# Kernel optimization log

Measured on AMD Instinct MI355X. Metric: run time of the kernel, lower is better.

The kernel has to match this reference:

```python
import jax, jax.numpy as jnp
import numpy as np

T, N, E, H = 10, 2048, 32768, 256
EPS = 1e-12  # F.normalize eps
COORDS_WEIGHT = 1.0


def setup_inputs() -> dict:
    key = jax.random.key(0)
    ks = jax.random.split(key, 16)

    def lin_w(k, fan_in, fan_out, gain=1.0):
        return (jax.random.normal(k, (fan_in, fan_out), jnp.float32)
                * gain / np.sqrt(fan_in)).astype(jnp.float32)

    return {
        "x": jax.random.normal(ks[0], (T, N, 4, 3), jnp.float32),
        "h": jax.random.normal(ks[1], (T, N, H), jnp.float32),
        "others": jax.random.normal(ks[2], (T, N, H), jnp.float32),
        # edge_mlp: Linear(2H+16 -> H), ReLU, Linear(H -> H), ReLU
        "We1": lin_w(ks[3], 2 * H + 16, H), "be1": jnp.zeros((H,), jnp.float32),
        "We2": lin_w(ks[4], H, H), "be2": jnp.zeros((H,), jnp.float32),
        # node_mlp: Linear(H + H + H -> H), ReLU, Linear(H -> H)
        "Wn1": lin_w(ks[5], 3 * H, H), "bn1": jnp.zeros((H,), jnp.float32),
        "Wn2": lin_w(ks[6], H, H), "bn2": jnp.zeros((H,), jnp.float32),
        # coord_mlp: Linear(H -> H), ReLU, Linear(H -> 1, bias=False, xavier gain 0.001)
        "Wc1": lin_w(ks[7], H, H), "bc1": jnp.zeros((H,), jnp.float32),
        "Wc2": lin_w(ks[8], H, 1, gain=0.001),
        "edge_index": jax.random.randint(ks[9], (2, E), 0, N, jnp.int64),
    }


def reference(x, h, others, We1, be1, We2, be2, Wn1, bn1, Wn2, bn2,
              Wc1, bc1, Wc2, edge_index):
    row, col = edge_index[0], edge_index[1]
    n_nodes = x.shape[1]

    # coord2radial (vectorized over the per-timestep python loop)
    coord_diff = x[:, row] - x[:, col]                      # [T,E,4,3]
    gram = jnp.einsum('tejd,tekd->tejk', coord_diff, coord_diff)
    gram = gram.reshape(gram.shape[0], gram.shape[1], 16)   # [T,E,16]
    radial = gram / jnp.maximum(
        jnp.linalg.norm(gram, axis=-1, keepdims=True), EPS)

    # edge_model: cat([source, target, radial]) -> MLP
    edge_in = jnp.concatenate([h[:, row], h[:, col], radial], axis=-1)
    e = jax.nn.relu(edge_in @ We1 + be1)
    e = jax.nn.relu(e @ We2 + be2)                          # [T,E,H]

    # coord_model: trans = coord_diff * coord_mlp(edge_feat)
    m = jax.nn.relu(e @ Wc1 + bc1) @ Wc2                    # [T,E,1]
    trans = coord_diff * m[..., None]                       # [T,E,4,3]

    seg_sum = lambda a: jax.vmap(
        lambda v: jax.ops.segment_sum(v, row, num_segments=n_nodes))(a)
    counts = jax.ops.segment_sum(
        jnp.ones((row.shape[0],), x.dtype), row, num_segments=n_nodes)
    counts = jnp.maximum(counts, 1.0)

    f = (seg_sum(trans) / counts[None, :, None, None]) * COORDS_WEIGHT
    coord_out = x + f                                       # [T,N,4,3]

    # node_model: agg = segment_sum(edge_feat, row); cat([others, h, agg])
    agg = seg_sum(e)                                        # [T,N,H]
    node_in = jnp.concatenate([others, h, agg], axis=-1)    # [T,N,3H]
    n_out = jax.nn.relu(node_in @ Wn1 + bn1) @ Wn2 + bn2
    h_out = h + n_out                                       # recurrent residual
    return h_out, coord_out
```

## Files before the change

kernel.cpp:

```cpp
#include <hip/hip_runtime.h>
#include <hip/hip_bf16.h>
#include <stdint.h>

#define TT 10
#define NN 2048
#define EE 32768
#define HH 256

typedef short bf16x8 __attribute__((ext_vector_type(8)));
typedef float f32x4 __attribute__((ext_vector_type(4)));

__device__ __forceinline__ float b2f(unsigned short u) {
    unsigned int x = ((unsigned int)u) << 16;
    return __builtin_bit_cast(float, x);
}
__device__ __forceinline__ unsigned short f2b(float f) {
    unsigned int x = __builtin_bit_cast(unsigned int, f);
    unsigned int r = x + 0x7FFFu + ((x >> 16) & 1u);
    return (unsigned short)(r >> 16);
}

#define GLOAD_LDS16(g, l)                                                      \
    __builtin_amdgcn_global_load_lds(                                          \
        (const __attribute__((address_space(1))) void*)(g),                    \
        (__attribute__((address_space(3))) void*)(l), 16, 0, 0)


__global__ void cvt_bf16_kernel(const float* __restrict__ in,
                                unsigned short* __restrict__ out, int n) {
    int i = blockIdx.x * blockDim.x + threadIdx.x;
    int stride = gridDim.x * blockDim.x;
    for (; i < n; i += stride) out[i] = f2b(in[i]);
}

__global__ void transpose_w_kernel(const float* __restrict__ W,
                                   unsigned short* __restrict__ Wt, int K, int KPAD) {
    int idx = blockIdx.x * blockDim.x + threadIdx.x;
    if (idx >= 256 * KPAD) return;
    int n = idx / KPAD, k = idx - n * KPAD;
    Wt[idx] = (k < K) ? f2b(W[k * 256 + n]) : (unsigned short)0;
}

__global__ void zero_f32_kernel(float* __restrict__ p, int n) {
    int i = blockIdx.x * blockDim.x + threadIdx.x;
    int stride = gridDim.x * blockDim.x;
    for (; i < n; i += stride) p[i] = 0.0f;
}

__global__ void count_kernel(const int* __restrict__ rows, int* __restrict__ counts) {
    int e = blockIdx.x * blockDim.x + threadIdx.x;
    if (e < EE) atomicAdd(&counts[rows[e]], 1);
}

__global__ __launch_bounds__(256) void scan_kernel(const int* __restrict__ counts,
                                                   int* __restrict__ boff) {
    __shared__ int part[256];
    int tid = threadIdx.x;
    int base = tid * 8;
    int local[8];
    int s = 0;
#pragma unroll
    for (int i = 0; i < 8; ++i) { local[i] = s; s += counts[base + i]; }
    part[tid] = s;
    __syncthreads();
    for (int offd = 1; offd < 256; offd <<= 1) {
        int v = (tid >= offd) ? part[tid - offd] : 0;
        __syncthreads();
        part[tid] += v;
        __syncthreads();
    }
    int pbase = (tid == 0) ? 0 : part[tid - 1];
#pragma unroll
    for (int i = 0; i < 8; ++i) boff[base + i] = pbase + local[i];
    if (tid == 255) boff[2048] = pbase + s;
}

__global__ void scatter_kernel(const int* __restrict__ rows, const int* __restrict__ cols,
                               const int* __restrict__ boff, int* __restrict__ cursor,
                               int* __restrict__ rs, int* __restrict__ cs) {
    int e = blockIdx.x * blockDim.x + threadIdx.x;
    if (e < EE) {
        int r = rows[e];
        int pos = boff[r] + atomicAdd(&cursor[r], 1);
        rs[pos] = r;
        cs[pos] = cols[e];
    }
}


__device__ __forceinline__ void stageB(const unsigned short* __restrict__ Wt,
                                       int KPAD, int k0, int tid, int w,
                                       unsigned short* Bs) {
    int trow = tid >> 3;
    int sk8 = ((tid & 7) ^ (trow & 7)) * 8;
#pragma unroll
    for (int i = 0; i < 8; ++i) {
        int row = i * 32 + trow;
        GLOAD_LDS16(Wt + (size_t)row * KPAD + k0 + sk8, Bs + i * 2048 + w * 512);
    }
}

__device__ __forceinline__ void mfma_step(const unsigned short* As,
                                          const unsigned short* Bs,
                                          int w, int lr, int lq, f32x4 acc[4][4]) {
    int xs = (lr & 7) << 3;
#pragma unroll
    for (int kk = 0; kk < 64; kk += 32) {
        bf16x8 a[4], b[4];
        int pc = (kk + lq * 8) ^ xs;
#pragma unroll
        for (int m = 0; m < 4; ++m)
            a[m] = *reinterpret_cast<const bf16x8*>(As + (m * 16 + lr) * 64 + pc);
#pragma unroll
        for (int n = 0; n < 4; ++n)
            b[n] = *reinterpret_cast<const bf16x8*>(
                Bs + (w * 64 + n * 16 + lr) * 64 + pc);
#pragma unroll
        for (int m = 0; m < 4; ++m)
#pragma unroll
            for (int n = 0; n < 4; ++n)
                acc[m][n] = __builtin_amdgcn_mfma_f32_16x16x32_bf16(
                    a[m], b[n], acc[m][n], 0, 0, 0);
    }
}

__device__ __forceinline__ void mfma_step_es(const unsigned short* Es,
                                             const unsigned short* Bs, int k0,
                                             int w, int lr, int lq, f32x4 acc[4][4]) {
    int xs = (lr & 7) << 3;
#pragma unroll
    for (int kk = 0; kk < 64; kk += 32) {
        bf16x8 a[4], b[4];
        int lcol = kk + lq * 8;
#pragma unroll
        for (int m = 0; m < 4; ++m)
            a[m] = *reinterpret_cast<const bf16x8*>(
                Es + (m * 16 + lr) * 256 + ((k0 + lcol) ^ xs));
#pragma unroll
        for (int n = 0; n < 4; ++n)
            b[n] = *reinterpret_cast<const bf16x8*>(
                Bs + (w * 64 + n * 16 + lr) * 64 + (lcol ^ xs));
#pragma unroll
        for (int m = 0; m < 4; ++m)
#pragma unroll
            for (int n = 0; n < 4; ++n)
                acc[m][n] = __builtin_amdgcn_mfma_f32_16x16x32_bf16(
                    a[m], b[n], acc[m][n], 0, 0, 0);
    }
}

__global__ __launch_bounds__(256, 2) void edge_mega_kernel(
    const float* __restrict__ x, const unsigned short* __restrict__ hb,
    const unsigned short* __restrict__ We1t, const float* __restrict__ be1,
    const unsigned short* __restrict__ We2t, const float* __restrict__ be2,
    const unsigned short* __restrict__ Wc1t, const float* __restrict__ bc1,
    const float* __restrict__ Wc2,
    const int* __restrict__ rs, const int* __restrict__ cs,
    float* __restrict__ aggf, float* __restrict__ csum) {
    __shared__ unsigned short As[64 * 64];
    __shared__ unsigned short Bs[256 * 64];
    __shared__ unsigned short Es[64 * 256];
    __shared__ float CDs[64][12];
    __shared__ unsigned short Rs[64][16];
    __shared__ float Ms[64][4];

    int tid = threadIdx.x;
    int lane = tid & 63, w = tid >> 6;
    int lr = lane & 15, lq = lane >> 4;
    int blockRow = blockIdx.x * 64;
    int tt = blockRow >> 15;
    int sb = blockRow & (EE - 1);

    if (tid < 64) {
        int s = sb + tid;
        int r = rs[s], c = cs[s];
        const float* xr = x + ((size_t)tt * NN + r) * 12;
        const float* xc = x + ((size_t)tt * NN + c) * 12;
        float cd[12];
#pragma unroll
        for (int i = 0; i < 12; ++i) {
            cd[i] = xr[i] - xc[i];
            CDs[tid][i] = cd[i];
        }
        float g[16], ss = 0.f;
#pragma unroll
        for (int j = 0; j < 4; ++j)
#pragma unroll
            for (int k = 0; k < 4; ++k) {
                float v = cd[j * 3] * cd[k * 3] + cd[j * 3 + 1] * cd[k * 3 + 1] +
                          cd[j * 3 + 2] * cd[k * 3 + 2];
                g[j * 4 + k] = v;
                ss += v * v;
            }
        float inv = 1.f / fmaxf(sqrtf(ss), 1e-12f);
#pragma unroll
        for (int i = 0; i < 16; ++i) Rs[tid][i] = f2b(g[i] * inv);
    }

    int trow = tid >> 3;
    int sk8 = ((tid & 7) ^ (trow & 7)) * 8;
    const unsigned short *hr0, *hc0, *hr1, *hc1;
    {
        int s0 = sb + trow;
        int s1 = sb + 32 + trow;
        hr0 = hb + ((size_t)tt * NN + rs[s0]) * 256 + sk8;
        hc0 = hb + ((size_t)tt * NN + cs[s0]) * 256 + sk8 - 256;
        hr1 = hb + ((size_t)tt * NN + rs[s1]) * 256 + sk8;
        hc1 = hb + ((size_t)tt * NN + cs[s1]) * 256 + sk8 - 256;
    }

    __syncthreads();

    f32x4 acc[4][4];
#pragma unroll
    for (int m = 0; m < 4; ++m)
#pragma unroll
        for (int n = 0; n < 4; ++n) acc[m][n] = (f32x4){0.f, 0.f, 0.f, 0.f};

#pragma unroll 1
    for (int k0 = 0; k0 < 512; k0 += 64) {
        const unsigned short* s0 = (k0 < 256) ? hr0 + k0 : hc0 + k0;
        const unsigned short* s1 = (k0 < 256) ? hr1 + k0 : hc1 + k0;
        GLOAD_LDS16(s0, As + w * 512);
        GLOAD_LDS16(s1, As + 2048 + w * 512);
        stageB(We1t, 576, k0, tid, w, Bs);
        __syncthreads();
        mfma_step(As, Bs, w, lr, lq, acc);
        __syncthreads();
    }
    {
#pragma unroll
        for (int j = 0; j < 2; ++j) {
            int row = j * 32 + trow;
            int lseg = (tid & 7) ^ (row & 7);
            bf16x8 v = {};
            if (lseg < 2) {
#pragma unroll
                for (int ii = 0; ii < 8; ++ii)
                    v[ii] = (short)Rs[row][lseg * 8 + ii];
            }
            *reinterpret_cast<bf16x8*>(As + row * 64 + (tid & 7) * 8) = v;
        }
        stageB(We1t, 576, 512, tid, w, Bs);
        __syncthreads();
        mfma_step(As, Bs, w, lr, lq, acc);
        __syncthreads();
    }
    {
        float bv[4];
#pragma unroll
        for (int n = 0; n < 4; ++n) bv[n] = be1[w * 64 + n * 16 + lr];
#pragma unroll
        for (int m = 0; m < 4; ++m)
#pragma unroll
            for (int r = 0; r < 4; ++r) {
                int row = m * 16 + lq * 4 + r;
                int xsw = (row & 7) << 3;
#pragma unroll
                for (int n = 0; n < 4; ++n) {
                    int col = w * 64 + n * 16 + lr;
                    float v = fmaxf(acc[m][n][r] + bv[n], 0.f);
                    Es[row * 256 + (col ^ xsw)] = f2b(v);
                }
            }
    }
    __syncthreads();

#pragma unroll
    for (int m = 0; m < 4; ++m)
#pragma unroll
        for (int n = 0; n < 4; ++n) acc[m][n] = (f32x4){0.f, 0.f, 0.f, 0.f};
#pragma unroll 1
    for (int k0 = 0; k0 < 256; k0 += 64) {
        stageB(We2t, 256, k0, tid, w, Bs);
        __syncthreads();
        mfma_step_es(Es, Bs, k0, w, lr, lq, acc);
        __syncthreads();
    }
    {
        float bv[4];
#pragma unroll
        for (int n = 0; n < 4; ++n) bv[n] = be2[w * 64 + n * 16 + lr];
#pragma unroll
        for (int m = 0; m < 4; ++m)
#pragma unroll
            for (int r = 0; r < 4; ++r) {
                int row = m * 16 + lq * 4 + r;
                int xsw = (row & 7) << 3;
#pragma unroll
                for (int n = 0; n < 4; ++n) {
                    int col = w * 64 + n * 16 + lr;
                    float v = fmaxf(acc[m][n][r] + bv[n], 0.f);
                    Es[row * 256 + (col ^ xsw)] = f2b(v);
                }
            }
    }
    __syncthreads();

#pragma unroll
    for (int m = 0; m < 4; ++m)
#pragma unroll
        for (int n = 0; n < 4; ++n) acc[m][n] = (f32x4){0.f, 0.f, 0.f, 0.f};
#pragma unroll 1
    for (int k0 = 0; k0 < 256; k0 += 64) {
        stageB(Wc1t, 256, k0, tid, w, Bs);
        __syncthreads();
        mfma_step_es(Es, Bs, k0, w, lr, lq, acc);
        __syncthreads();
    }
    {
        float bv[4], wv[4];
#pragma unroll
        for (int n = 0; n < 4; ++n) {
            int col = w * 64 + n * 16 + lr;
            bv[n] = bc1[col];
            wv[n] = Wc2[col];
        }
#pragma unroll
        for (int m = 0; m < 4; ++m)
#pragma unroll
            for (int r = 0; r < 4; ++r) {
                float p = 0.f;
#pragma unroll
                for (int n = 0; n < 4; ++n)
                    p += fmaxf(acc[m][n][r] + bv[n], 0.f) * wv[n];
                p += __shfl_xor(p, 1);
                p += __shfl_xor(p, 2);
                p += __shfl_xor(p, 4);
                p += __shfl_xor(p, 8);
                if (lr == 0) Ms[m * 16 + lq * 4 + r][w] = p;
            }
    }
    __syncthreads();

    if (tid < 64) {
        Ms[tid][0] = Ms[tid][0] + Ms[tid][1] + Ms[tid][2] + Ms[tid][3];
    }
    __syncthreads();

    {
        float accv = 0.f;
        for (int i = 0; i < 64; ++i) {
            int ncur = rs[sb + i];
            accv += b2f(Es[i * 256 + (tid ^ ((i & 7) << 3))]);
            if (i == 63 || rs[sb + i + 1] != ncur) {
                atomicAdd(&aggf[((size_t)tt * NN + ncur) * 256 + tid], accv);
                accv = 0.f;
            }
        }
    }
    if (tid < 12) {
        float a = 0.f;
        for (int i = 0; i < 64; ++i) {
            int ncur = rs[sb + i];
            a += CDs[i][tid] * Ms[i][0];
            if (i == 63 || rs[sb + i + 1] != ncur) {
                atomicAdd(&csum[((size_t)tt * NN + ncur) * 12 + tid], a);
                a = 0.f;
            }
        }
    }
}

template<int EPI>
__global__ __launch_bounds__(256) void gemm_kernel(
    const unsigned short* __restrict__ A, const unsigned short* __restrict__ Wt,
    const float* __restrict__ bias, unsigned short* __restrict__ Cb, int KPAD,
    const float* __restrict__ resid, float* __restrict__ outf) {
    __shared__ unsigned short As[128 * 32];
    __shared__ unsigned short Bs[128 * 32];
    int tid = threadIdx.x;
    int lane = tid & 63, w = tid >> 6;
    int wr = w >> 1, wc = w & 1;
    int blockRow = blockIdx.x * 128, colBase = blockIdx.y * 128;
    int l4 = lane >> 2;
    int seg = lane & 3;

    int ar0 = blockRow + w * 16 + l4;
    int br0 = colBase + w * 16 + l4;
    const unsigned short* pA0 = A + (size_t)ar0 * KPAD + seg * 8;
    const unsigned short* pA1 = pA0 + (size_t)64 * KPAD;
    const unsigned short* pB0 = Wt + (size_t)br0 * KPAD + seg * 8;
    const unsigned short* pB1 = pB0 + (size_t)64 * KPAD;

    unsigned short* ldsA = As + w * 512;
    unsigned short* ldsB = Bs + w * 512;

    f32x4 acc[4][4] = {};
    int lr = lane & 15, lq = lane >> 4;

    for (int k0 = 0; k0 < KPAD; k0 += 32) {
        GLOAD_LDS16(pA0 + k0, ldsA);
        GLOAD_LDS16(pA1 + k0, ldsA + 2048);
        GLOAD_LDS16(pB0 + k0, ldsB);
        GLOAD_LDS16(pB1 + k0, ldsB + 2048);
        __syncthreads();
        bf16x8 a[4], b[4];
#pragma unroll
        for (int m = 0; m < 4; ++m)
            a[m] = *reinterpret_cast<const bf16x8*>(
                As + (wr * 64 + m * 16 + lr) * 32 + lq * 8);
#pragma unroll
        for (int n = 0; n < 4; ++n)
            b[n] = *reinterpret_cast<const bf16x8*>(
                Bs + (wc * 64 + n * 16 + lr) * 32 + lq * 8);
#pragma unroll
        for (int m = 0; m < 4; ++m)
#pragma unroll
            for (int n = 0; n < 4; ++n)
                acc[m][n] = __builtin_amdgcn_mfma_f32_16x16x32_bf16(
                    a[m], b[n], acc[m][n], 0, 0, 0);
        __syncthreads();
    }

    float bv[4];
#pragma unroll
    for (int n = 0; n < 4; ++n) bv[n] = bias[colBase + wc * 64 + n * 16 + lr];

#pragma unroll
    for (int m = 0; m < 4; ++m)
#pragma unroll
        for (int r = 0; r < 4; ++r) {
            int row = blockRow + wr * 64 + m * 16 + lq * 4 + r;
#pragma unroll
            for (int n = 0; n < 4; ++n) {
                int col = colBase + wc * 64 + n * 16 + lr;
                float v = acc[m][n][r] + bv[n];
                if (EPI == 2) {
                    outf[(size_t)row * 256 + col] =
                        v + resid[(size_t)row * 256 + col];
                } else {
                    Cb[(size_t)row * 256 + col] = f2b(fmaxf(v, 0.f));
                }
            }
        }
}

__global__ void nodein_kernel(const float* __restrict__ others,
                              const unsigned short* __restrict__ hb,
                              const float* __restrict__ aggf,
                              unsigned short* __restrict__ node_in) {
    int idx = blockIdx.x * blockDim.x + threadIdx.x;
    int stride = gridDim.x * blockDim.x;
    const int total = TT * NN * 192;
    for (; idx < total; idx += stride) {
        int nf = idx / 192, c4 = (idx - nf * 192) * 4;
        ushort4 v;
        if (c4 < 256) {
            float4 o = *reinterpret_cast<const float4*>(others + (size_t)nf * 256 + c4);
            v.x = f2b(o.x); v.y = f2b(o.y); v.z = f2b(o.z); v.w = f2b(o.w);
        } else if (c4 < 512) {
            v = *reinterpret_cast<const ushort4*>(hb + (size_t)nf * 256 + (c4 - 256));
        } else {
            float4 a = *reinterpret_cast<const float4*>(aggf + (size_t)nf * 256 + (c4 - 512));
            v.x = f2b(a.x); v.y = f2b(a.y); v.z = f2b(a.z); v.w = f2b(a.w);
        }
        *reinterpret_cast<ushort4*>(node_in + (size_t)nf * 768 + c4) = v;
    }
}

__global__ void coordout_kernel(const float* __restrict__ x, const int* __restrict__ counts,
                                const float* __restrict__ csum, float* __restrict__ outc) {
    int idx = blockIdx.x * blockDim.x + threadIdx.x;
    if (idx >= TT * NN * 12) return;
    int n = (idx / 12) & (NN - 1);
    float cnt = (float)(counts[n] > 0 ? counts[n] : 1);
    outc[idx] = x[idx] + csum[idx] / cnt;
}


extern "C" void kernel_launch(void* const* d_in, const int* in_sizes, int n_in,
                              void* d_out, int out_size, void* d_ws, size_t ws_size,
                              hipStream_t stream) {
    const float* x = (const float*)d_in[0];
    const float* h = (const float*)d_in[1];
    const float* others = (const float*)d_in[2];
    const float* We1 = (const float*)d_in[3];
    const float* be1 = (const float*)d_in[4];
    const float* We2 = (const float*)d_in[5];
    const float* be2 = (const float*)d_in[6];
    const float* Wn1 = (const float*)d_in[7];
    const float* bn1 = (const float*)d_in[8];
    const float* Wn2 = (const float*)d_in[9];
    const float* bn2 = (const float*)d_in[10];
    const float* Wc1 = (const float*)d_in[11];
    const float* bc1 = (const float*)d_in[12];
    const float* Wc2 = (const float*)d_in[13];
    const int* ei = (const int*)d_in[14];
    const int* rows = ei;
    const int* cols = ei + EE;

    char* wsb = (char*)d_ws;
    size_t off = 0;
    auto alloc = [&](size_t bytes) {
        void* p = wsb + off;
        off = (off + bytes + 255) & ~(size_t)255;
        return p;
    };
    const int TNH = TT * NN * HH;
    unsigned short* hb = (unsigned short*)alloc((size_t)TNH * 2);
    unsigned short* We1t = (unsigned short*)alloc(256 * 576 * 2);
    unsigned short* We2t = (unsigned short*)alloc(256 * 256 * 2);
    unsigned short* Wn1t = (unsigned short*)alloc(256 * 768 * 2);
    unsigned short* Wn2t = (unsigned short*)alloc(256 * 256 * 2);
    unsigned short* Wc1t = (unsigned short*)alloc(256 * 256 * 2);
    float* aggf = (float*)alloc((size_t)TT * NN * 256 * 4);
    float* csum = (float*)alloc((size_t)TT * NN * 12 * 4);
    int* counts = (int*)alloc((size_t)2048 * 4);
    int* cursor = (int*)alloc((size_t)2048 * 4);
    int* boff = (int*)alloc((size_t)2049 * 4);
    int* rs = (int*)alloc((size_t)EE * 4);
    int* cs = (int*)alloc((size_t)EE * 4);
    unsigned short* node_in = (unsigned short*)alloc((size_t)TT * NN * 768 * 2);
    unsigned short* Z = (unsigned short*)alloc((size_t)TT * NN * 256 * 2);
    (void)ws_size;

    cvt_bf16_kernel<<<2048, 256, 0, stream>>>(h, hb, TNH);
    transpose_w_kernel<<<576, 256, 0, stream>>>(We1, We1t, 528, 576);
    transpose_w_kernel<<<256, 256, 0, stream>>>(We2, We2t, 256, 256);
    transpose_w_kernel<<<768, 256, 0, stream>>>(Wn1, Wn1t, 768, 768);
    transpose_w_kernel<<<256, 256, 0, stream>>>(Wn2, Wn2t, 256, 256);
    transpose_w_kernel<<<256, 256, 0, stream>>>(Wc1, Wc1t, 256, 256);
    zero_f32_kernel<<<16, 256, 0, stream>>>((float*)counts, 4096);
    count_kernel<<<EE / 256, 256, 0, stream>>>(rows, counts);
    scan_kernel<<<1, 256, 0, stream>>>(counts, boff);
    scatter_kernel<<<EE / 256, 256, 0, stream>>>(rows, cols, boff, cursor, rs, cs);
    zero_f32_kernel<<<2048, 256, 0, stream>>>(aggf, TT * NN * 256 + TT * NN * 12);

    float* houtf = (float*)d_out;
    float* coutf = (float*)d_out + (size_t)TT * NN * HH;

    edge_mega_kernel<<<TT * EE / 64, 256, 0, stream>>>(
        x, hb, We1t, be1, We2t, be2, Wc1t, bc1, Wc2, rs, cs, aggf, csum);

    nodein_kernel<<<2048, 256, 0, stream>>>(others, hb, aggf, node_in);
    gemm_kernel<0><<<dim3(TT * NN / 128, 2), 256, 0, stream>>>(
        node_in, Wn1t, bn1, Z, 768, nullptr, nullptr);
    gemm_kernel<2><<<dim3(TT * NN / 128, 2), 256, 0, stream>>>(
        Z, Wn2t, bn2, nullptr, 256, h, houtf);

    coordout_kernel<<<(TT * NN * 12 + 255) / 256, 256, 0, stream>>>(
        x, counts, csum, coutf);
}
```

Before: 406.0 us.

## Double-buffer edge MLP GEMMs with 128-edge tiles and 512-thread blocks

Restructures the fused edge kernel to process 128 edges per block using 8 waves arranged 2x4, with K-step 32 and double-buffered LDS staging so global loads of the next K slice overlap MFMA on the current one. The padded K of We1 shrinks from 576 to 544 to drop wasted radial padding work. This halves the per-tile weight reload traffic relative to edges and removes one barrier per step, at the cost of higher LDS use (about 1 block per CU) and a larger register/occupancy tradeoff.

Result: slower. 518.8 us (+27.8%).

```diff
diff --git a/kernel.cpp b/kernel.cpp
--- a/kernel.cpp
+++ b/kernel.cpp
@@ -87,69 +87,7 @@
     }
 }
 
-
-__device__ __forceinline__ void stageB(const unsigned short* __restrict__ Wt,
-                                       int KPAD, int k0, int tid, int w,
-                                       unsigned short* Bs) {
-    int trow = tid >> 3;
-    int sk8 = ((tid & 7) ^ (trow & 7)) * 8;
-#pragma unroll
-    for (int i = 0; i < 8; ++i) {
-        int row = i * 32 + trow;
-        GLOAD_LDS16(Wt + (size_t)row * KPAD + k0 + sk8, Bs + i * 2048 + w * 512);
-    }
-}
-
-__device__ __forceinline__ void mfma_step(const unsigned short* As,
-                                          const unsigned short* Bs,
-                                          int w, int lr, int lq, f32x4 acc[4][4]) {
-    int xs = (lr & 7) << 3;
-#pragma unroll
-    for (int kk = 0; kk < 64; kk += 32) {
-        bf16x8 a[4], b[4];
-        int pc = (kk + lq * 8) ^ xs;
-#pragma unroll
-        for (int m = 0; m < 4; ++m)
-            a[m] = *reinterpret_cast<const bf16x8*>(As + (m * 16 + lr) * 64 + pc);
-#pragma unroll
-        for (int n = 0; n < 4; ++n)
-            b[n] = *reinterpret_cast<const bf16x8*>(
-                Bs + (w * 64 + n * 16 + lr) * 64 + pc);
-#pragma unroll
-        for (int m = 0; m < 4; ++m)
-#pragma unroll
-            for (int n = 0; n < 4; ++n)
-                acc[m][n] = __builtin_amdgcn_mfma_f32_16x16x32_bf16(
-                    a[m], b[n], acc[m][n], 0, 0, 0);
-    }
-}
-
-__device__ __forceinline__ void mfma_step_es(const unsigned short* Es,
-                                             const unsigned short* Bs, int k0,
-                                             int w, int lr, int lq, f32x4 acc[4][4]) {
-    int xs = (lr & 7) << 3;
-#pragma unroll
-    for (int kk = 0; kk < 64; kk += 32) {
-        bf16x8 a[4], b[4];
-        int lcol = kk + lq * 8;
-#pragma unroll
-        for (int m = 0; m < 4; ++m)
-            a[m] = *reinterpret_cast<const bf16x8*>(
-                Es + (m * 16 + lr) * 256 + ((k0 + lcol) ^ xs));
-#pragma unroll
-        for (int n = 0; n < 4; ++n)
-            b[n] = *reinterpret_cast<const bf16x8*>(
-                Bs + (w * 64 + n * 16 + lr) * 64 + (lcol ^ xs));
-#pragma unroll
-        for (int m = 0; m < 4; ++m)
-#pragma unroll
-            for (int n = 0; n < 4; ++n)
-                acc[m][n] = __builtin_amdgcn_mfma_f32_16x16x32_bf16(
-                    a[m], b[n], acc[m][n], 0, 0, 0);
-    }
-}
-
-__global__ __launch_bounds__(256, 2) void edge_mega_kernel(
+__global__ __launch_bounds__(512, 1) void edge_mega_kernel(
     const float* __restrict__ x, const unsigned short* __restrict__ hb,
     const unsigned short* __restrict__ We1t, const float* __restrict__ be1,
     const unsigned short* __restrict__ We2t, const float* __restrict__ be2,
@@ -157,21 +95,22 @@
     const float* __restrict__ Wc2,
     const int* __restrict__ rs, const int* __restrict__ cs,
     float* __restrict__ aggf, float* __restrict__ csum) {
-    __shared__ unsigned short As[64 * 64];
-    __shared__ unsigned short Bs[256 * 64];
-    __shared__ unsigned short Es[64 * 256];
-    __shared__ float CDs[64][12];
-    __shared__ unsigned short Rs[64][16];
-    __shared__ float Ms[64][4];
+    __shared__ unsigned short As[2 * 128 * 32];
+    __shared__ unsigned short Bs[2 * 256 * 32];
+    __shared__ unsigned short Es[128 * 256];
+    __shared__ float CDs[128][12];
+    __shared__ unsigned short Rs[128][16];
+    __shared__ float Ms[128][4];
 
     int tid = threadIdx.x;
     int lane = tid & 63, w = tid >> 6;
+    int wr = w >> 2, wc = w & 3;
     int lr = lane & 15, lq = lane >> 4;
-    int blockRow = blockIdx.x * 64;
+    int blockRow = blockIdx.x * 128;
     int tt = blockRow >> 15;
     int sb = blockRow & (EE - 1);
 
-    if (tid < 64) {
+    if (tid < 128) {
         int s = sb + tid;
         int r = rs[s], c = cs[s];
         const float* xr = x + ((size_t)tt * NN + r) * 12;
@@ -197,19 +136,15 @@
         for (int i = 0; i < 16; ++i) Rs[tid][i] = f2b(g[i] * inv);
     }
 
-    int trow = tid >> 3;
-    int sk8 = ((tid & 7) ^ (trow & 7)) * 8;
-    const unsigned short *hr0, *hc0, *hr1, *hc1;
+    int srow = tid >> 2, sslot = tid & 3;
+    int xoff = ((sslot ^ (srow & 3)) * 8);
+    const unsigned short *hrp, *hcp;
     {
-        int s0 = sb + trow;
-        int s1 = sb + 32 + trow;
-        hr0 = hb + ((size_t)tt * NN + rs[s0]) * 256 + sk8;
-        hc0 = hb + ((size_t)tt * NN + cs[s0]) * 256 + sk8 - 256;
-        hr1 = hb + ((size_t)tt * NN + rs[s1]) * 256 + sk8;
-        hc1 = hb + ((size_t)tt * NN + cs[s1]) * 256 + sk8 - 256;
-    }
-
-    __syncthreads();
+        int ir = rs[sb + srow], ic = cs[sb + srow];
+        hrp = hb + ((size_t)tt * NN + ir) * 256 + xoff;
+        hcp = hb + ((size_t)tt * NN + ic) * 256 + xoff - 256;
+    }
+    int axoff = (lq ^ (lr & 3)) * 8;
 
     f32x4 acc[4][4];
 #pragma unroll
@@ -217,145 +152,178 @@
 #pragma unroll
         for (int n = 0; n < 4; ++n) acc[m][n] = (f32x4){0.f, 0.f, 0.f, 0.f};
 
-#pragma unroll 1
-    for (int k0 = 0; k0 < 512; k0 += 64) {
-        const unsigned short* s0 = (k0 < 256) ? hr0 + k0 : hc0 + k0;
-        const unsigned short* s1 = (k0 < 256) ? hr1 + k0 : hc1 + k0;
-        GLOAD_LDS16(s0, As + w * 512);
-        GLOAD_LDS16(s1, As + 2048 + w * 512);
-        stageB(We1t, 576, k0, tid, w, Bs);
-        __syncthreads();
-        mfma_step(As, Bs, w, lr, lq, acc);
-        __syncthreads();
-    }
-    {
-#pragma unroll
-        for (int j = 0; j < 2; ++j) {
-            int row = j * 32 + trow;
-            int lseg = (tid & 7) ^ (row & 7);
-            bf16x8 v = {};
-            if (lseg < 2) {
-#pragma unroll
-                for (int ii = 0; ii < 8; ++ii)
-                    v[ii] = (short)Rs[row][lseg * 8 + ii];
-            }
-            *reinterpret_cast<bf16x8*>(As + row * 64 + (tid & 7) * 8) = v;
-        }
-        stageB(We1t, 576, 512, tid, w, Bs);
-        __syncthreads();
-        mfma_step(As, Bs, w, lr, lq, acc);
-        __syncthreads();
-    }
-    {
+    auto stageB = [&](const unsigned short* Wt, int KPAD, int buf, int k0) {
+        GLOAD_LDS16(Wt + (size_t)srow * KPAD + k0 + xoff, Bs + buf * 8192 + w * 512);
+        GLOAD_LDS16(Wt + (size_t)(128 + srow) * KPAD + k0 + xoff,
+                    Bs + buf * 8192 + 4096 + w * 512);
+    };
+    auto mfma32 = [&](int buf) {
+        const unsigned short* Ab = As + buf * 4096;
+        const unsigned short* Bb = Bs + buf * 8192;
+        bf16x8 a[4], b[4];
+#pragma unroll
+        for (int m = 0; m < 4; ++m)
+            a[m] = *reinterpret_cast<const bf16x8*>(
+                Ab + (wr * 64 + m * 16 + lr) * 32 + axoff);
+#pragma unroll
+        for (int n = 0; n < 4; ++n)
+            b[n] = *reinterpret_cast<const bf16x8*>(
+                Bb + (wc * 64 + n * 16 + lr) * 32 + axoff);
+#pragma unroll
+        for (int m = 0; m < 4; ++m)
+#pragma unroll
+            for (int n = 0; n < 4; ++n)
+                acc[m][n] = __builtin_amdgcn_mfma_f32_16x16x32_bf16(
+                    a[m], b[n], acc[m][n], 0, 0, 0);
+    };
+    auto mfma_es = [&](int buf, int k0) {
+        const unsigned short* Bb = Bs + buf * 8192;
+        int ex = (k0 + lq * 8) ^ ((lr & 7) << 3);
+        bf16x8 a[4], b[4];
+#pragma unroll
+        for (int m = 0; m < 4; ++m)
+            a[m] = *reinterpret_cast<const bf16x8*>(
+                Es + (wr * 64 + m * 16 + lr) * 256 + ex);
+#pragma unroll
+        for (int n = 0; n < 4; ++n)
+            b[n] = *reinterpret_cast<const bf16x8*>(
+                Bb + (wc * 64 + n * 16 + lr) * 32 + axoff);
+#pragma unroll
+        for (int m = 0; m < 4; ++m)
+#pragma unroll
+            for (int n = 0; n < 4; ++n)
+                acc[m][n] = __builtin_amdgcn_mfma_f32_16x16x32_bf16(
+                    a[m], b[n], acc[m][n], 0, 0, 0);
+    };
+    auto epi_es = [&](const float* __restrict__ bias) {
         float bv[4];
 #pragma unroll
-        for (int n = 0; n < 4; ++n) bv[n] = be1[w * 64 + n * 16 + lr];
-#pragma unroll
-        for (int m = 0; m < 4; ++m)
-#pragma unroll
-            for (int r = 0; r < 4; ++r) {
-                int row = m * 16 + lq * 4 + r;
+        for (int n = 0; n < 4; ++n) bv[n] = bias[wc * 64 + n * 16 + lr];
+#pragma unroll
+        for (int m = 0; m < 4; ++m)
+#pragma unroll
+            for (int rr = 0; rr < 4; ++rr) {
+                int row = wr * 64 + m * 16 + lq * 4 + rr;
                 int xsw = (row & 7) << 3;
 #pragma unroll
                 for (int n = 0; n < 4; ++n) {
-                    int col = w * 64 + n * 16 + lr;
-                    float v = fmaxf(acc[m][n][r] + bv[n], 0.f);
+                    int col = wc * 64 + n * 16 + lr;
+                    float v = fmaxf(acc[m][n][rr] + bv[n], 0.f);
                     Es[row * 256 + (col ^ xsw)] = f2b(v);
                 }
             }
+    };
+    auto acc_reset = [&]() {
+#pragma unroll
+        for (int m = 0; m < 4; ++m)
+#pragma unroll
+            for (int n = 0; n < 4; ++n) acc[m][n] = (f32x4){0.f, 0.f, 0.f, 0.f};
+    };
+
+    {
+        GLOAD_LDS16(hrp, As + w * 512);
+        stageB(We1t, 544, 0, 0);
+        int cur = 0;
+        for (int s = 0; s < 17; ++s) {
+            __syncthreads();
+            int nxt = cur ^ 1;
+            if (s < 15) {
+                const unsigned short* sa =
+                    (s + 1 < 8) ? hrp + 32 * (s + 1) : hcp + 32 * (s + 1);
+                GLOAD_LDS16(sa, As + nxt * 4096 + w * 512);
+                stageB(We1t, 544, nxt, 32 * (s + 1));
+            } else if (s == 15) {
+                int ls = sslot ^ (srow & 3);
+                bf16x8 v = {};
+                if (ls < 2) {
+#pragma unroll
+                    for (int ii = 0; ii < 8; ++ii)
+                        v[ii] = (short)Rs[srow][ls * 8 + ii];
+                }
+                *reinterpret_cast<bf16x8*>(As + nxt * 4096 + tid * 8) = v;
+                stageB(We1t, 544, nxt, 512);
+            }
+            mfma32(cur);
+            cur ^= 1;
+        }
     }
     __syncthreads();
-
-#pragma unroll
-    for (int m = 0; m < 4; ++m)
-#pragma unroll
-        for (int n = 0; n < 4; ++n) acc[m][n] = (f32x4){0.f, 0.f, 0.f, 0.f};
-#pragma unroll 1
-    for (int k0 = 0; k0 < 256; k0 += 64) {
-        stageB(We2t, 256, k0, tid, w, Bs);
-        __syncthreads();
-        mfma_step_es(Es, Bs, k0, w, lr, lq, acc);
-        __syncthreads();
-    }
+    stageB(We2t, 256, 0, 0);
+    epi_es(be1);
+
+    acc_reset();
     {
-        float bv[4];
-#pragma unroll
-        for (int n = 0; n < 4; ++n) bv[n] = be2[w * 64 + n * 16 + lr];
-#pragma unroll
-        for (int m = 0; m < 4; ++m)
-#pragma unroll
-            for (int r = 0; r < 4; ++r) {
-                int row = m * 16 + lq * 4 + r;
-                int xsw = (row & 7) << 3;
-#pragma unroll
-                for (int n = 0; n < 4; ++n) {
-                    int col = w * 64 + n * 16 + lr;
-                    float v = fmaxf(acc[m][n][r] + bv[n], 0.f);
-                    Es[row * 256 + (col ^ xsw)] = f2b(v);
-                }
-            }
+        int cur = 0;
+        for (int s = 0; s < 8; ++s) {
+            __syncthreads();
+            if (s < 7) stageB(We2t, 256, cur ^ 1, 32 * (s + 1));
+            mfma_es(cur, 32 * s);
+            cur ^= 1;
+        }
     }
     __syncthreads();
-
-#pragma unroll
-    for (int m = 0; m < 4; ++m)
-#pragma unroll
-        for (int n = 0; n < 4; ++n) acc[m][n] = (f32x4){0.f, 0.f, 0.f, 0.f};
-#pragma unroll 1
-    for (int k0 = 0; k0 < 256; k0 += 64) {
-        stageB(Wc1t, 256, k0, tid, w, Bs);
-        __syncthreads();
-        mfma_step_es(Es, Bs, k0, w, lr, lq, acc);
-        __syncthreads();
+    stageB(Wc1t, 256, 0, 0);
+    epi_es(be2);
+
+    acc_reset();
+    {
+        int cur = 0;
+        for (int s = 0; s < 8; ++s) {
+            __syncthreads();
+            if (s < 7) stageB(Wc1t, 256, cur ^ 1, 32 * (s + 1));
+            mfma_es(cur, 32 * s);
+            cur ^= 1;
+        }
     }
     {
         float bv[4], wv[4];
 #pragma unroll
         for (int n = 0; n < 4; ++n) {
-            int col = w * 64 + n * 16 + lr;
+            int col = wc * 64 + n * 16 + lr;
             bv[n] = bc1[col];
             wv[n] = Wc2[col];
         }
 #pragma unroll
         for (int m = 0; m < 4; ++m)
 #pragma unroll
-            for (int r = 0; r < 4; ++r) {
+            for (int rr = 0; rr < 4; ++rr) {
                 float p = 0.f;
 #pragma unroll
                 for (int n = 0; n < 4; ++n)
-                    p += fmaxf(acc[m][n][r] + bv[n], 0.f) * wv[n];
+                    p += fmaxf(acc[m][n][rr] + bv[n], 0.f) * wv[n];
                 p += __shfl_xor(p, 1);
                 p += __shfl_xor(p, 2);
                 p += __shfl_xor(p, 4);
                 p += __shfl_xor(p, 8);
-                if (lr == 0) Ms[m * 16 + lq * 4 + r][w] = p;
+                if (lr == 0) Ms[wr * 64 + m * 16 + lq * 4 + rr][wc] = p;
             }
     }
     __syncthreads();
-
-    if (tid < 64) {
-        Ms[tid][0] = Ms[tid][0] + Ms[tid][1] + Ms[tid][2] + Ms[tid][3];
-    }
+    if (tid < 128) Ms[tid][0] += Ms[tid][1] + Ms[tid][2] + Ms[tid][3];
     __syncthreads();
 
     {
+        int colw = tid & 255;
+        int i0 = (tid >> 8) * 64;
         float accv = 0.f;
-        for (int i = 0; i < 64; ++i) {
+        for (int i = i0; i < i0 + 64; ++i) {
             int ncur = rs[sb + i];
-            accv += b2f(Es[i * 256 + (tid ^ ((i & 7) << 3))]);
-            if (i == 63 || rs[sb + i + 1] != ncur) {
-                atomicAdd(&aggf[((size_t)tt * NN + ncur) * 256 + tid], accv);
+            accv += b2f(Es[i * 256 + (colw ^ ((i & 7) << 3))]);
+            if (i == i0 + 63 || rs[sb + i + 1] != ncur) {
+                atomicAdd(&aggf[((size_t)tt * NN + ncur) * 256 + colw], accv);
                 accv = 0.f;
             }
         }
     }
-    if (tid < 12) {
+    if (tid < 24) {
+        int g = tid / 12, c = tid - g * 12;
+        int i0 = g * 64;
         float a = 0.f;
-        for (int i = 0; i < 64; ++i) {
+        for (int i = i0; i < i0 + 64; ++i) {
             int ncur = rs[sb + i];
-            a += CDs[i][tid] * Ms[i][0];
-            if (i == 63 || rs[sb + i + 1] != ncur) {
-                atomicAdd(&csum[((size_t)tt * NN + ncur) * 12 + tid], a);
+            a += CDs[i][c] * Ms[i][0];
+            if (i == i0 + 63 || rs[sb + i + 1] != ncur) {
+                atomicAdd(&csum[((size_t)tt * NN + ncur) * 12 + c], a);
                 a = 0.f;
             }
         }
@@ -499,7 +467,7 @@
     };
     const int TNH = TT * NN * HH;
     unsigned short* hb = (unsigned short*)alloc((size_t)TNH * 2);
-    unsigned short* We1t = (unsigned short*)alloc(256 * 576 * 2);
+    unsigned short* We1t = (unsigned short*)alloc(256 * 544 * 2);
     unsigned short* We2t = (unsigned short*)alloc(256 * 256 * 2);
     unsigned short* Wn1t = (unsigned short*)alloc(256 * 768 * 2);
     unsigned short* Wn2t = (unsigned short*)alloc(256 * 256 * 2);
@@ -516,7 +484,7 @@
     (void)ws_size;
 
     cvt_bf16_kernel<<<2048, 256, 0, stream>>>(h, hb, TNH);
-    transpose_w_kernel<<<576, 256, 0, stream>>>(We1, We1t, 528, 576);
+    transpose_w_kernel<<<544, 256, 0, stream>>>(We1, We1t, 528, 544);
     transpose_w_kernel<<<256, 256, 0, stream>>>(We2, We2t, 256, 256);
     transpose_w_kernel<<<768, 256, 0, stream>>>(Wn1, Wn1t, 768, 768);
     transpose_w_kernel<<<256, 256, 0, stream>>>(Wn2, Wn2t, 256, 256);
@@ -530,7 +498,7 @@
     float* houtf = (float*)d_out;
     float* coutf = (float*)d_out + (size_t)TT * NN * HH;
 
-    edge_mega_kernel<<<TT * EE / 64, 256, 0, stream>>>(
+    edge_mega_kernel<<<TT * EE / 128, 512, 0, stream>>>(
         x, hb, We1t, be1, We2t, be2, Wc1t, bc1, Wc2, rs, cs, aggf, csum);
 
     nodein_kernel<<<2048, 256, 0, stream>>>(others, hb, aggf, node_in);
```

## Precompute per-node first-layer projections instead of per-edge gathered GEMM

Applied to the files above, without the earlier changes.

Splits the first edge-MLP layer so the source and target halves of We1 are applied once per node via two dense GEMMs (Ya = h@We1a + be1, Yb = h@We1b). The edge kernel then gathers these fp32 projections per edge and adds them in the epilogue, leaving only the small radial K=64 MFMA step per edge. This cuts first-layer FLOPs by the edge/node ratio (16x) but adds two extra GEMM launches, fp32 intermediate buffers, and uncoalesced scattered fp32 gathers in the epilogue. Weight transposes are also merged into one kernel launch.

Result: faster. 358.7 us (-11.7%).

```diff
diff --git a/kernel.cpp b/kernel.cpp
--- a/kernel.cpp
+++ b/kernel.cpp
@@ -33,12 +33,45 @@
     for (; i < n; i += stride) out[i] = f2b(in[i]);
 }
 
-__global__ void transpose_w_kernel(const float* __restrict__ W,
-                                   unsigned short* __restrict__ Wt, int K, int KPAD) {
+__global__ void transpose_all_kernel(
+    const float* __restrict__ We1, const float* __restrict__ We2,
+    const float* __restrict__ Wn1, const float* __restrict__ Wn2,
+    const float* __restrict__ Wc1,
+    unsigned short* __restrict__ We1at, unsigned short* __restrict__ We1bt,
+    unsigned short* __restrict__ Wrt, unsigned short* __restrict__ We2t,
+    unsigned short* __restrict__ Wn1t, unsigned short* __restrict__ Wn2t,
+    unsigned short* __restrict__ Wc1t) {
     int idx = blockIdx.x * blockDim.x + threadIdx.x;
-    if (idx >= 256 * KPAD) return;
-    int n = idx / KPAD, k = idx - n * KPAD;
-    Wt[idx] = (k < K) ? f2b(W[k * 256 + n]) : (unsigned short)0;
+    const int s1 = 65536;
+    const int s2 = s1 + 65536;
+    const int s3 = s2 + 16384;
+    const int s4 = s3 + 65536;
+    const int s5 = s4 + 196608;
+    const int s6 = s5 + 65536;
+    const int s7 = s6 + 65536;
+    if (idx >= s7) return;
+    if (idx < s1) {
+        int li = idx, n = li >> 8, k = li & 255;
+        We1at[li] = f2b(We1[k * 256 + n]);
+    } else if (idx < s2) {
+        int li = idx - s1, n = li >> 8, k = li & 255;
+        We1bt[li] = f2b(We1[(256 + k) * 256 + n]);
+    } else if (idx < s3) {
+        int li = idx - s2, n = li >> 6, k = li & 63;
+        Wrt[li] = (k < 16) ? f2b(We1[(512 + k) * 256 + n]) : (unsigned short)0;
+    } else if (idx < s4) {
+        int li = idx - s3, n = li >> 8, k = li & 255;
+        We2t[li] = f2b(We2[k * 256 + n]);
+    } else if (idx < s5) {
+        int li = idx - s4, n = li / 768, k = li - n * 768;
+        Wn1t[li] = f2b(Wn1[k * 256 + n]);
+    } else if (idx < s6) {
+        int li = idx - s5, n = li >> 8, k = li & 255;
+        Wn2t[li] = f2b(Wn2[k * 256 + n]);
+    } else {
+        int li = idx - s6, n = li >> 8, k = li & 255;
+        Wc1t[li] = f2b(Wc1[k * 256 + n]);
+    }
 }
 
 __global__ void zero_f32_kernel(float* __restrict__ p, int n) {
@@ -150,8 +183,9 @@
 }
 
 __global__ __launch_bounds__(256, 2) void edge_mega_kernel(
-    const float* __restrict__ x, const unsigned short* __restrict__ hb,
-    const unsigned short* __restrict__ We1t, const float* __restrict__ be1,
+    const float* __restrict__ x,
+    const float* __restrict__ Ya, const float* __restrict__ Yb,
+    const unsigned short* __restrict__ Wrt,
     const unsigned short* __restrict__ We2t, const float* __restrict__ be2,
     const unsigned short* __restrict__ Wc1t, const float* __restrict__ bc1,
     const float* __restrict__ Wc2,
@@ -198,16 +232,6 @@
     }
 
     int trow = tid >> 3;
-    int sk8 = ((tid & 7) ^ (trow & 7)) * 8;
-    const unsigned short *hr0, *hc0, *hr1, *hc1;
-    {
-        int s0 = sb + trow;
-        int s1 = sb + 32 + trow;
-        hr0 = hb + ((size_t)tt * NN + rs[s0]) * 256 + sk8;
-        hc0 = hb + ((size_t)tt * NN + cs[s0]) * 256 + sk8 - 256;
-        hr1 = hb + ((size_t)tt * NN + rs[s1]) * 256 + sk8;
-        hc1 = hb + ((size_t)tt * NN + cs[s1]) * 256 + sk8 - 256;
-    }
 
     __syncthreads();
 
@@ -217,17 +241,6 @@
 #pragma unroll
         for (int n = 0; n < 4; ++n) acc[m][n] = (f32x4){0.f, 0.f, 0.f, 0.f};
 
-#pragma unroll 1
-    for (int k0 = 0; k0 < 512; k0 += 64) {
-        const unsigned short* s0 = (k0 < 256) ? hr0 + k0 : hc0 + k0;
-        const unsigned short* s1 = (k0 < 256) ? hr1 + k0 : hc1 + k0;
-        GLOAD_LDS16(s0, As + w * 512);
-        GLOAD_LDS16(s1, As + 2048 + w * 512);
-        stageB(We1t, 576, k0, tid, w, Bs);
-        __syncthreads();
-        mfma_step(As, Bs, w, lr, lq, acc);
-        __syncthreads();
-    }
     {
 #pragma unroll
         for (int j = 0; j < 2; ++j) {
@@ -241,25 +254,26 @@
             }
             *reinterpret_cast<bf16x8*>(As + row * 64 + (tid & 7) * 8) = v;
         }
-        stageB(We1t, 576, 512, tid, w, Bs);
+        stageB(Wrt, 64, 0, tid, w, Bs);
         __syncthreads();
         mfma_step(As, Bs, w, lr, lq, acc);
         __syncthreads();
     }
     {
-        float bv[4];
-#pragma unroll
-        for (int n = 0; n < 4; ++n) bv[n] = be1[w * 64 + n * 16 + lr];
 #pragma unroll
         for (int m = 0; m < 4; ++m)
 #pragma unroll
             for (int r = 0; r < 4; ++r) {
                 int row = m * 16 + lq * 4 + r;
+                int e = sb + row;
+                int ar = rs[e], ac = cs[e];
+                const float* pa = Ya + ((size_t)tt * NN + ar) * 256;
+                const float* pb = Yb + ((size_t)tt * NN + ac) * 256;
                 int xsw = (row & 7) << 3;
 #pragma unroll
                 for (int n = 0; n < 4; ++n) {
                     int col = w * 64 + n * 16 + lr;
-                    float v = fmaxf(acc[m][n][r] + bv[n], 0.f);
+                    float v = fmaxf(acc[m][n][r] + pa[col] + pb[col], 0.f);
                     Es[row * 256 + (col ^ xsw)] = f2b(v);
                 }
             }
@@ -429,6 +443,8 @@
                 if (EPI == 2) {
                     outf[(size_t)row * 256 + col] =
                         v + resid[(size_t)row * 256 + col];
+                } else if (EPI == 1) {
+                    outf[(size_t)row * 256 + col] = v;
                 } else {
                     Cb[(size_t)row * 256 + col] = f2b(fmaxf(v, 0.f));
                 }
@@ -499,15 +515,20 @@
     };
     const int TNH = TT * NN * HH;
     unsigned short* hb = (unsigned short*)alloc((size_t)TNH * 2);
-    unsigned short* We1t = (unsigned short*)alloc(256 * 576 * 2);
+    unsigned short* We1at = (unsigned short*)alloc(256 * 256 * 2);
+    unsigned short* We1bt = (unsigned short*)alloc(256 * 256 * 2);
+    unsigned short* Wrt = (unsigned short*)alloc(256 * 64 * 2);
     unsigned short* We2t = (unsigned short*)alloc(256 * 256 * 2);
     unsigned short* Wn1t = (unsigned short*)alloc(256 * 768 * 2);
     unsigned short* Wn2t = (unsigned short*)alloc(256 * 256 * 2);
     unsigned short* Wc1t = (unsigned short*)alloc(256 * 256 * 2);
+    float* Ya = (float*)alloc((size_t)TNH * 4);
+    float* Yb = (float*)alloc((size_t)TNH * 4);
     float* aggf = (float*)alloc((size_t)TT * NN * 256 * 4);
     float* csum = (float*)alloc((size_t)TT * NN * 12 * 4);
     int* counts = (int*)alloc((size_t)2048 * 4);
     int* cursor = (int*)alloc((size_t)2048 * 4);
+    float* zeros256 = (float*)alloc((size_t)256 * 4);
     int* boff = (int*)alloc((size_t)2049 * 4);
     int* rs = (int*)alloc((size_t)EE * 4);
     int* cs = (int*)alloc((size_t)EE * 4);
@@ -516,12 +537,9 @@
     (void)ws_size;
 
     cvt_bf16_kernel<<<2048, 256, 0, stream>>>(h, hb, TNH);
-    transpose_w_kernel<<<576, 256, 0, stream>>>(We1, We1t, 528, 576);
-    transpose_w_kernel<<<256, 256, 0, stream>>>(We2, We2t, 256, 256);
-    transpose_w_kernel<<<768, 256, 0, stream>>>(Wn1, Wn1t, 768, 768);
-    transpose_w_kernel<<<256, 256, 0, stream>>>(Wn2, Wn2t, 256, 256);
-    transpose_w_kernel<<<256, 256, 0, stream>>>(Wc1, Wc1t, 256, 256);
-    zero_f32_kernel<<<16, 256, 0, stream>>>((float*)counts, 4096);
+    transpose_all_kernel<<<2112, 256, 0, stream>>>(
+        We1, We2, Wn1, Wn2, Wc1, We1at, We1bt, Wrt, We2t, Wn1t, Wn2t, Wc1t);
+    zero_f32_kernel<<<17, 256, 0, stream>>>((float*)counts, 4096 + 256);
     count_kernel<<<EE / 256, 256, 0, stream>>>(rows, counts);
     scan_kernel<<<1, 256, 0, stream>>>(counts, boff);
     scatter_kernel<<<EE / 256, 256, 0, stream>>>(rows, cols, boff, cursor, rs, cs);
@@ -530,8 +548,13 @@
     float* houtf = (float*)d_out;
     float* coutf = (float*)d_out + (size_t)TT * NN * HH;
 
+    gemm_kernel<1><<<dim3(TT * NN / 128, 2), 256, 0, stream>>>(
+        hb, We1at, be1, nullptr, 256, nullptr, Ya);
+    gemm_kernel<1><<<dim3(TT * NN / 128, 2), 256, 0, stream>>>(
+        hb, We1bt, zeros256, nullptr, 256, nullptr, Yb);
+
     edge_mega_kernel<<<TT * EE / 64, 256, 0, stream>>>(
-        x, hb, We1t, be1, We2t, be2, Wc1t, bc1, Wc2, rs, cs, aggf, csum);
+        x, Ya, Yb, Wrt, We2t, be2, Wc1t, bc1, Wc2, rs, cs, aggf, csum);
 
     nodein_kernel<<<2048, 256, 0, stream>>>(others, hb, aggf, node_in);
     gemm_kernel<0><<<dim3(TT * NN / 128, 2), 256, 0, stream>>>(
```
